# Kernel tuning notes

Hardware: AMD Instinct MI355X
Metric: run time of the kernel (lower is better)

Reference implementation:

```python
import jax, jax.numpy as jnp
import numpy as np

HIDDEN = 768
HEADS = 12
HEAD_DIM = 64
SEQ = 512
DS_K = 64  # downsampling_k
EPS = 1e-6


def setup_inputs() -> dict:
    key = jax.random.key(0)
    ks = jax.random.split(key, 16)
    B = 32
    sd = 1.0 / DS_K
    glorot = jax.nn.initializers.lecun_normal()  # flax default_kernel_init
    inp = {
        "query": jax.random.normal(ks[0], (B, SEQ, HIDDEN), jnp.float32),
        "key": jax.random.normal(ks[1], (B, SEQ, HIDDEN), jnp.float32),
        "value": jax.random.normal(ks[2], (B, SEQ, HIDDEN), jnp.float32),
        "step": 0,
        # learned Linformer-style downsampling projections [k, s]
        "W_kds": sd * jax.random.normal(ks[3], (DS_K, SEQ), jnp.float32),
        "W_vds": sd * jax.random.normal(ks[4], (DS_K, SEQ), jnp.float32),
        # DenseGeneral qkv kernels [d, n, h] and biases [n, h]
        "Wq": glorot(ks[5], (HIDDEN, HEADS, HEAD_DIM), jnp.float32),
        "bq": jnp.zeros((HEADS, HEAD_DIM), jnp.float32),
        "Wk": glorot(ks[6], (HIDDEN, HEADS, HEAD_DIM), jnp.float32),
        "bk": jnp.zeros((HEADS, HEAD_DIM), jnp.float32),
        "Wv": glorot(ks[7], (HIDDEN, HEADS, HEAD_DIM), jnp.float32),
        "bv": jnp.zeros((HEADS, HEAD_DIM), jnp.float32),
        # out projection contracts (n, h) -> hidden
        "Wout": glorot(ks[8], (HEADS * HEAD_DIM, HIDDEN), jnp.float32).reshape(HEADS, HEAD_DIM, HIDDEN),
        "bout": jnp.zeros((HIDDEN,), jnp.float32),
    }
    return inp


def reference(query, key, value, step, W_kds, W_vds, Wq, bq, Wk, bk, Wv, bv, Wout, bout):
    # Linformer-style downsample of keys/values along sequence: [b,s,d] -> [b,k,d]
    key_ds = jnp.einsum("ks,bsd->bkd", W_kds, key)
    val_ds = jnp.einsum("ks,bsd->bkd", W_vds, value)

    # per-head projections
    queries = jnp.einsum("bqd,dnh->bqnh", query, Wq) + bq    # [b,q,n,h]
    keys = jnp.einsum("bkd,dnh->bknh", key_ds, Wk) + bk      # [b,k,n,h]
    values = jnp.einsum("bkd,dnh->bknh", val_ds, Wv) + bv    # [b,k,n,h]

    # kernelized linear attention with elu feature map (mask=False path)
    phi_q = jax.nn.elu(queries) + 1.0
    phi_k = jax.nn.elu(keys) + 1.0
    s = jnp.einsum("bknd,bknh->bndh", phi_k, values)          # [b,n,h,h] KV state
    z = jnp.sum(phi_k, axis=1)                                 # [b,n,h]
    qs = jnp.einsum("bqnd,bndh->bqnh", phi_q, s)
    qz = jnp.einsum("bqnd,bnd->bqn", phi_q, z) + EPS
    a_v = qs / qz[..., None]                                   # [b,q,n,h]

    out = jnp.einsum("bqnh,nhD->bqD", a_v, Wout) + bout        # [b,q,hidden]
    return out
```

## Files before the change

### kernel.cpp

```cpp
#include <hip/hip_runtime.h>

typedef unsigned short u16;
typedef u16 u16x4 __attribute__((ext_vector_type(4)));
typedef u16 u16x8 __attribute__((ext_vector_type(8)));
typedef __bf16 bf16;
typedef bf16 bf16x8 __attribute__((ext_vector_type(8)));
typedef float f32x4 __attribute__((ext_vector_type(4)));

__device__ __forceinline__ float bf2f(u16 v) {
  union { unsigned u; float f; } x; x.u = ((unsigned)v) << 16; return x.f;
}
__device__ __forceinline__ u16 f2bf(float f) {
  union { float f; unsigned u; } x; x.f = f;
  unsigned u = x.u;
  u += 0x7fffu + ((u >> 16) & 1u);
  return (u16)(u >> 16);
}
__device__ __forceinline__ unsigned cvt2bf(float lo, float hi) {
  unsigned r;
  asm("v_cvt_pk_bf16_f32 %0, %1, %2" : "=v"(r) : "v"(lo), "v"(hi));
  return r;
}

__device__ __forceinline__ void bar_lgkm() {
  asm volatile("s_waitcnt lgkmcnt(0)" ::: "memory");
  __builtin_amdgcn_s_barrier();
}

#define GLDS16(g, l) __builtin_amdgcn_global_load_lds( \
    (const __attribute__((address_space(1))) unsigned int*)(const void*)(g), \
    (__attribute__((address_space(3))) unsigned int*)(void*)(l), 16, 0, 0)

__global__ __launch_bounds__(256) void prepds_k(
    const float* __restrict__ Wq, const float* __restrict__ Wk,
    const float* __restrict__ Wv, const float* __restrict__ Wout,
    const float* __restrict__ query,
    const float* __restrict__ W_kds, const float* __restrict__ W_vds,
    const float* __restrict__ b0, const float* __restrict__ b1,
    const float* __restrict__ b2, const float* __restrict__ b3,
    const float* __restrict__ key, const float* __restrict__ value,
    u16* __restrict__ WT, u16* __restrict__ q_bf,
    u16* __restrict__ dstB, u16* __restrict__ key_ds)
{
  __shared__ char sm[10240];
  const int blk = blockIdx.x;
  const int t = threadIdx.x;

  if (blk % 10 == 0) {
    u16* Bs = (u16*)sm;
    const int id = blk / 10;
    const int nt = (id % 12) * 64;
    const int yb = id / 12;
    const int pair = yb >> 5, b = yb & 31;
    const float* src = (pair ? value : key) + (size_t)b * 512 * 768;
    const float* W32 = pair ? W_vds : W_kds;
    u16* dst = key_ds + (size_t)pair * 1572864 + (size_t)b * 49152;
    const int wave = t >> 6, lane = t & 63;
    const int wm = (wave >> 1) * 32, wn = (wave & 1) * 32;
    const int lrow = lane & 15, quad = lane >> 4;
    const int bn = t & 63, bk8 = (t >> 6) * 8;
    const float* bcol = src + nt + bn;

    auto ldW = [&](int row, int kq) -> bf16x8 {
      f32x4 w0 = *(const f32x4*)&W32[(size_t)row * 512 + kq];
      f32x4 w1 = *(const f32x4*)&W32[(size_t)row * 512 + kq + 4];
      union { unsigned u[4]; bf16x8 v; } cv;
      cv.u[0] = cvt2bf(w0[0], w0[1]); cv.u[1] = cvt2bf(w0[2], w0[3]);
      cv.u[2] = cvt2bf(w1[0], w1[1]); cv.u[3] = cvt2bf(w1[2], w1[3]);
      return cv.v;
    };

    f32x4 acc[2][2] = {};
    float breg[8];
    bf16x8 av[2][2];

    #pragma unroll
    for (int i = 0; i < 8; ++i) breg[i] = bcol[(size_t)(bk8 + i) * 768];
    #pragma unroll
    for (int i = 0; i < 2; ++i) av[0][i] = ldW(wm + i * 16 + lrow, quad * 8);

    #pragma unroll
    for (int step = 0; step < 16; ++step) {
      const int cur = step & 1, nxt = cur ^ 1;
      u16x8 wv;
      #pragma unroll
      for (int i = 0; i < 8; ++i) wv[i] = f2bf(breg[i]);
      *(u16x8*)&Bs[cur * 2560 + bn * 40 + bk8] = wv;
      if (step < 15) {
        const int k1 = (step + 1) * 32;
        #pragma unroll
        for (int i = 0; i < 8; ++i) breg[i] = bcol[(size_t)(k1 + bk8 + i) * 768];
        #pragma unroll
        for (int i = 0; i < 2; ++i) av[nxt][i] = ldW(wm + i * 16 + lrow, k1 + quad * 8);
      }
      bar_lgkm();
      bf16x8 bv[2];
      #pragma unroll
      for (int j = 0; j < 2; ++j)
        bv[j] = *(const bf16x8*)&Bs[cur * 2560 + (wn + j * 16 + lrow) * 40 + quad * 8];
      #pragma unroll
      for (int i = 0; i < 2; ++i)
        #pragma unroll
        for (int j = 0; j < 2; ++j)
          acc[i][j] = __builtin_amdgcn_mfma_f32_16x16x32_bf16(av[cur][i], bv[j], acc[i][j], 0, 0, 0);
    }

    #pragma unroll
    for (int i = 0; i < 2; ++i)
      #pragma unroll
      for (int j = 0; j < 2; ++j) {
        const int col = nt + wn + j * 16 + lrow;
        #pragma unroll
        for (int r = 0; r < 4; ++r) {
          const int row = wm + i * 16 + quad * 4 + r;
          dst[(size_t)row * 768 + col] = f2bf(acc[i][j][r]);
        }
      }
    return;
  }

  const int pid = blk - blk / 10 - 1;
  if (pid < 576) {
    u16 (*T)[72] = (u16(*)[72])sm;
    const int bz = pid / 144, rr = pid % 144;
    const int r0 = (rr / 12) * 64, c0 = (rr % 12) * 64;
    const float* W = (bz == 0) ? Wq : (bz == 1) ? Wk : (bz == 2) ? Wv : Wout;
    u16* O = WT + (size_t)bz * 768 * 768;
    #pragma unroll
    for (int p = 0; p < 2; ++p) {
      int v = t + p * 256;
      int r = v / 8, c = (v % 8) * 8;
      f32x4 x0 = *(const f32x4*)&W[(size_t)(r0 + r) * 768 + c0 + c];
      f32x4 x1 = *(const f32x4*)&W[(size_t)(r0 + r) * 768 + c0 + c + 4];
      #pragma unroll
      for (int i = 0; i < 4; ++i) { T[r][c + i] = f2bf(x0[i]); T[r][c + 4 + i] = f2bf(x1[i]); }
    }
    __syncthreads();
    #pragma unroll
    for (int p = 0; p < 2; ++p) {
      int v = t + p * 256;
      int r = v / 8, c = (v % 8) * 8;
      u16x8 tv;
      #pragma unroll
      for (int i = 0; i < 8; ++i) tv[i] = T[c + i][r];
      *(u16x8*)&O[(size_t)(c0 + r) * 768 + r0 + c] = tv;
    }
  } else if (pid < 6720) {
    const size_t i = (size_t)(pid - 576) * 256 + t;
    f32x4 a = *(const f32x4*)&query[i * 8];
    f32x4 b = *(const f32x4*)&query[i * 8 + 4];
    u16x8 w;
    #pragma unroll
    for (int j = 0; j < 4; ++j) { w[j] = f2bf(a[j]); w[4 + j] = f2bf(b[j]); }
    *(u16x8*)&q_bf[i * 8] = w;
  } else if (pid < 6732) {
    const int i = (pid - 6720) * 256 + t;
    if (i < 3072) {
      int s = i / 768, si = i % 768;
      const float* src = (s == 0) ? b0 : (s == 1) ? b1 : (s == 2) ? b2 : b3;
      dstB[i] = f2bf(src[si]);
    }
  }
}

template<int ACT, bool OF32>
__global__ __launch_bounds__(256) void gemm64_k(
    const u16* __restrict__ A, int lda,
    const u16* __restrict__ Bt, int ldb,
    void* __restrict__ Craw, int ldc,
    const u16* __restrict__ bias, int K)
{
  __shared__ u16 As[128 * 64];
  __shared__ u16 Bs[128 * 64];
  const int blk = blockIdx.x;
  const int wg = (blk & 7) * 96 + (blk >> 3);
  const int mt = (wg / 6) * 128, nt = (wg % 6) * 128;
  const int t = threadIdx.x, wave = t >> 6, lane = t & 63;
  const int wm = (wave >> 1) * 64, wn = (wave & 1) * 64;
  const int lrow = lane & 15, quad = lane >> 4;
  f32x4 acc[4][4] = {};

  for (int k0 = 0; k0 < K; k0 += 64) {
    __syncthreads();
    #pragma unroll
    for (int p = 0; p < 4; ++p) {
      const int slot = wave * 256 + p * 64 + lane;
      const int r = slot >> 3, ch = slot & 7;
      const int chs = ch ^ (r & 7);
      const int lb = (wave * 256 + p * 64) * 8;
      GLDS16(&A[(size_t)(mt + r) * lda + k0 + chs * 8], &As[lb]);
      GLDS16(&Bt[(size_t)(nt + r) * ldb + k0 + chs * 8], &Bs[lb]);
    }
    __syncthreads();

    #pragma unroll
    for (int c = 0; c < 2; ++c) {
      bf16x8 av[4], bv[4];
      #pragma unroll
      for (int i = 0; i < 4; ++i) {
        const int row = wm + i * 16 + lrow;
        av[i] = *(const bf16x8*)&As[row * 64 + (((c * 4 + quad) ^ (row & 7)) * 8)];
      }
      #pragma unroll
      for (int j = 0; j < 4; ++j) {
        const int row = wn + j * 16 + lrow;
        bv[j] = *(const bf16x8*)&Bs[row * 64 + (((c * 4 + quad) ^ (row & 7)) * 8)];
      }
      #pragma unroll
      for (int i = 0; i < 4; ++i)
        #pragma unroll
        for (int j = 0; j < 4; ++j)
          acc[i][j] = __builtin_amdgcn_mfma_f32_16x16x32_bf16(av[i], bv[j], acc[i][j], 0, 0, 0);
    }
  }

  #pragma unroll
  for (int i = 0; i < 4; ++i) {
    #pragma unroll
    for (int j = 0; j < 4; ++j) {
      const int col = nt + wn + j * 16 + lrow;
      const float badd = bias ? bf2f(bias[col]) : 0.0f;
      #pragma unroll
      for (int r = 0; r < 4; ++r) {
        const int row = mt + wm + i * 16 + quad * 4 + r;
        float v = acc[i][j][r] + badd;
        if constexpr (ACT == 1) v = v > 0.0f ? v + 1.0f : __expf(v);
        if constexpr (OF32) ((float*)Craw)[(size_t)row * ldc + col] = v;
        else                ((u16*)Craw)[(size_t)row * ldc + col] = f2bf(v);
      }
    }
  }
}

__global__ __launch_bounds__(256) void fkv_k(
    const u16* __restrict__ key_ds,
    const u16* __restrict__ WT,
    const u16* __restrict__ bias_c,
    u16* __restrict__ sT, float* __restrict__ z)
{
  __shared__ char sm[32768];
  u16* T0 = (u16*)sm;
  u16* Pt = (u16*)sm;
  u16* Vt = (u16*)(sm + 9216);
  const int x = blockIdx.x;
  const int b = x / 12, n = x % 12;
  const int t = threadIdx.x, wave = t >> 6, lane = t & 63;
  const u16* srcs[4] = {
    key_ds + (size_t)b * 49152,
    WT + 589824 + (size_t)n * 49152,
    key_ds + 1572864 + (size_t)b * 49152,
    WT + 2 * 589824 + (size_t)n * 49152 };
  const int grow = lane >> 3;
  const int gchunk = (lane & 7) ^ (grow & 7);
  const int isV = wave & 1;
  const int wm = (wave >> 1) * 32;
  u16* Atile = T0 + (isV ? 2 : 0) * 4096;
  u16* Btile = T0 + (isV ? 3 : 1) * 4096;
  const int lrow = lane & 15, quad = lane >> 4;
  f32x4 acc[2][4] = {};

  for (int k0 = 0; k0 < 768; k0 += 64) {
    const u16* s = srcs[wave];
    u16* dtile = T0 + wave * 4096;
    #pragma unroll
    for (int j = 0; j < 8; ++j) {
      const u16* gsrc = s + (size_t)(j * 8 + grow) * 768 + k0 + gchunk * 8;
      GLDS16(gsrc, (char*)dtile + j * 1024);
    }
    __syncthreads();
    #pragma unroll
    for (int c = 0; c < 2; ++c) {
      bf16x8 av[2], bv[4];
      #pragma unroll
      for (int i = 0; i < 2; ++i) {
        const int row = wm + i * 16 + lrow;
        av[i] = *(const bf16x8*)&Atile[row * 64 + (((c * 4 + quad) ^ (row & 7)) * 8)];
      }
      #pragma unroll
      for (int j = 0; j < 4; ++j) {
        const int row = j * 16 + lrow;
        bv[j] = *(const bf16x8*)&Btile[row * 64 + (((c * 4 + quad) ^ (row & 7)) * 8)];
      }
      #pragma unroll
      for (int i = 0; i < 2; ++i)
        #pragma unroll
        for (int j = 0; j < 4; ++j)
          acc[i][j] = __builtin_amdgcn_mfma_f32_16x16x32_bf16(av[i], bv[j], acc[i][j], 0, 0, 0);
    }
    __syncthreads();
  }

  const u16* bias = bias_c + (isV ? 1536 : 768) + n * 64;
  u16* Ttile = isV ? Vt : Pt;
  #pragma unroll
  for (int i = 0; i < 2; ++i)
    #pragma unroll
    for (int j = 0; j < 4; ++j) {
      const int col = j * 16 + lrow;
      const float badd = bf2f(bias[col]);
      u16x4 pk4;
      #pragma unroll
      for (int r = 0; r < 4; ++r) {
        float v = acc[i][j][r] + badd;
        if (!isV) v = v > 0.0f ? v + 1.0f : __expf(v);
        pk4[r] = f2bf(v);
      }
      *(u16x4*)&Ttile[col * 72 + wm + i * 16 + quad * 4] = pk4;
    }
  __syncthreads();

  const int wm2 = (wave >> 1) * 32, wn2 = (wave & 1) * 32;
  f32x4 a2[2][2] = {};
  #pragma unroll
  for (int c = 0; c < 2; ++c) {
    bf16x8 av[2], bv[2];
    #pragma unroll
    for (int i = 0; i < 2; ++i)
      av[i] = *(const bf16x8*)&Vt[(wm2 + i * 16 + lrow) * 72 + c * 32 + quad * 8];
    #pragma unroll
    for (int j = 0; j < 2; ++j)
      bv[j] = *(const bf16x8*)&Pt[(wn2 + j * 16 + lrow) * 72 + c * 32 + quad * 8];
    #pragma unroll
    for (int i = 0; i < 2; ++i)
      #pragma unroll
      for (int j = 0; j < 2; ++j)
        a2[i][j] = __builtin_amdgcn_mfma_f32_16x16x32_bf16(av[i], bv[j], a2[i][j], 0, 0, 0);
  }
  u16* sTg = sT + (size_t)x * 4096;
  #pragma unroll
  for (int i = 0; i < 2; ++i)
    #pragma unroll
    for (int j = 0; j < 2; ++j)
      #pragma unroll
      for (int r = 0; r < 4; ++r)
        sTg[(size_t)(wm2 + i * 16 + quad * 4 + r) * 64 + wn2 + j * 16 + lrow] = f2bf(a2[i][j][r]);
  if (t < 64) {
    float zz = 0.f;
    #pragma unroll
    for (int g = 0; g < 8; ++g) {
      u16x8 p = *(const u16x8*)&Pt[t * 72 + g * 8];
      #pragma unroll
      for (int e = 0; e < 8; ++e) zz += bf2f(p[e]);
    }
    z[(size_t)x * 64 + t] = zz;
  }
}

__global__ __launch_bounds__(256) void attn_av_k(
    u16* __restrict__ phi_q, const u16* __restrict__ sT, const float* __restrict__ zbuf)
{
  __shared__ u16 As[64 * 72];
  __shared__ u16 Bs[64 * 72];
  __shared__ float zv[64];
  __shared__ float zpart[4][64];
  __shared__ float zq[64];
  const int x = blockIdx.x, y = blockIdx.y;
  const int b = y / 12, n = y % 12;
  const int t = threadIdx.x;
  u16* Abase = phi_q + (size_t)b * 512 * 768 + (size_t)x * 64 * 768 + n * 64;
  const u16* Bbase = sT + (size_t)y * 4096;
  if (t < 64) zv[t] = zbuf[(size_t)y * 64 + t];
  #pragma unroll
  for (int p = 0; p < 2; ++p) {
    int v = t + p * 256;
    int r = v >> 3, c = (v & 7) * 8;
    *(u16x8*)&As[r * 72 + c] = *(const u16x8*)&Abase[(size_t)r * 768 + c];
    *(u16x8*)&Bs[r * 72 + c] = *(const u16x8*)&Bbase[r * 64 + c];
  }
  __syncthreads();
  {
    int r = t & 63, seg = t >> 6;
    float s = 0.f;
    #pragma unroll
    for (int j = 0; j < 16; ++j) s += bf2f(As[r * 72 + seg * 16 + j]) * zv[seg * 16 + j];
    zpart[seg][r] = s;
  }
  __syncthreads();
  if (t < 64) {
    float s = zpart[0][t] + zpart[1][t] + zpart[2][t] + zpart[3][t];
    zq[t] = 1.0f / (s + 1e-6f);
  }
  const int wave = t >> 6, lane = t & 63;
  const int wm = (wave >> 1) * 32, wn = (wave & 1) * 32;
  const int lrow = lane & 15, quad = lane >> 4;
  f32x4 acc[2][2] = {};
  #pragma unroll
  for (int c = 0; c < 2; ++c) {
    bf16x8 av[2], bv[2];
    #pragma unroll
    for (int i = 0; i < 2; ++i) av[i] = *(const bf16x8*)&As[(wm + i * 16 + lrow) * 72 + c * 32 + quad * 8];
    #pragma unroll
    for (int j = 0; j < 2; ++j) bv[j] = *(const bf16x8*)&Bs[(wn + j * 16 + lrow) * 72 + c * 32 + quad * 8];
    #pragma unroll
    for (int i = 0; i < 2; ++i)
      #pragma unroll
      for (int j = 0; j < 2; ++j)
        acc[i][j] = __builtin_amdgcn_mfma_f32_16x16x32_bf16(av[i], bv[j], acc[i][j], 0, 0, 0);
  }
  __syncthreads();
  #pragma unroll
  for (int i = 0; i < 2; ++i)
    #pragma unroll
    for (int j = 0; j < 2; ++j) {
      const int col = wn + j * 16 + lrow;
      #pragma unroll
      for (int r = 0; r < 4; ++r) {
        const int row = wm + i * 16 + quad * 4 + r;
        Abase[(size_t)row * 768 + col] = f2bf(acc[i][j][r] * zq[row]);
      }
    }
}

__global__ void tagfill_k(float* out, float val, int n) {
  int i = blockIdx.x * 256 + threadIdx.x;
  if (i < n) out[i] = val;
}

extern "C" void kernel_launch(void* const* d_in, const int* in_sizes, int n_in,
                              void* d_out, int out_size, void* d_ws, size_t ws_size,
                              hipStream_t stream) {
  (void)out_size;
  float* out = (float*)d_out;

  int o;
  if (n_in >= 14 && in_sizes[3] == 1) o = 4;
  else if (n_in == 13) o = 3;
  else { tagfill_k<<<4, 256, 0, stream>>>(out, 77.0f, 1024); return; }
  if (in_sizes[0] != 12582912 || in_sizes[o + 0] != 32768 || in_sizes[o + 2] != 589824) {
    tagfill_k<<<4, 256, 0, stream>>>(out, 88.0f, 1024); return;
  }

  const float* query = (const float*)d_in[0];
  const float* key   = (const float*)d_in[1];
  const float* value = (const float*)d_in[2];
  const float* W_kds = (const float*)d_in[o + 0];
  const float* W_vds = (const float*)d_in[o + 1];
  const float* Wq   = (const float*)d_in[o + 2];
  const float* bq   = (const float*)d_in[o + 3];
  const float* Wk   = (const float*)d_in[o + 4];
  const float* bk   = (const float*)d_in[o + 5];
  const float* Wv   = (const float*)d_in[o + 6];
  const float* bv   = (const float*)d_in[o + 7];
  const float* Wout = (const float*)d_in[o + 8];
  const float* bout = (const float*)d_in[o + 9];

  const size_t NEED = 61478912;
  if (ws_size < NEED) { tagfill_k<<<4, 256, 0, stream>>>(out, 123.0f, 1024); return; }

  char* base = (char*)d_ws;
  u16*   WT     = (u16*)base;
  char*  Breg   = base + 4718592;
  u16*   q_bf   = (u16*)Breg;
  u16*   sT     = (u16*)Breg;
  float* zbuf   = (float*)(Breg + 3145728);
  u16*   phi_q  = (u16*)(base + 29884416);
  u16*   bias_c = (u16*)(base + 55181312);
  u16*   key_ds = (u16*)(base + 55187456);
  u16* a_v = phi_q;
  u16* WqT   = WT;
  u16* WoutT = WT + 3 * 768 * 768;
  u16* bq_c = bias_c, *bout_c = bias_c + 2304;

  prepds_k<<<7680, 256, 0, stream>>>(Wq, Wk, Wv, Wout, query, W_kds, W_vds,
                                     bq, bk, bv, bout, key, value,
                                     WT, q_bf, bias_c, key_ds);

  gemm64_k<1, false><<<768, 256, 0, stream>>>(
      q_bf, 768, WqT, 768, phi_q, 768, bq_c, 768);

  fkv_k<<<384, 256, 0, stream>>>(key_ds, WT, bias_c, sT, zbuf);

  attn_av_k<<<dim3(8, 384), 256, 0, stream>>>(phi_q, sT, zbuf);

  gemm64_k<0, true><<<768, 256, 0, stream>>>(
      a_v, 768, WoutT, 768, out, 768, bout_c, 768);
}
```

Baseline: 319.7 us.

## Split sequence downsampling into its own kernel with smaller tiles and bf16 weights

```diff
diff --git a/kernel.cpp b/kernel.cpp
--- a/kernel.cpp
+++ b/kernel.cpp
@@ -16,11 +16,6 @@
   u += 0x7fffu + ((u >> 16) & 1u);
   return (u16)(u >> 16);
 }
-__device__ __forceinline__ unsigned cvt2bf(float lo, float hi) {
-  unsigned r;
-  asm("v_cvt_pk_bf16_f32 %0, %1, %2" : "=v"(r) : "v"(lo), "v"(hi));
-  return r;
-}
 
 __device__ __forceinline__ void bar_lgkm() {
   asm volatile("s_waitcnt lgkmcnt(0)" ::: "memory");
@@ -31,98 +26,21 @@
     (const __attribute__((address_space(1))) unsigned int*)(const void*)(g), \
     (__attribute__((address_space(3))) unsigned int*)(void*)(l), 16, 0, 0)
 
-__global__ __launch_bounds__(256) void prepds_k(
+__global__ __launch_bounds__(256) void prep_k(
     const float* __restrict__ Wq, const float* __restrict__ Wk,
     const float* __restrict__ Wv, const float* __restrict__ Wout,
     const float* __restrict__ query,
-    const float* __restrict__ W_kds, const float* __restrict__ W_vds,
+    const float* __restrict__ wkds, const float* __restrict__ wvds,
     const float* __restrict__ b0, const float* __restrict__ b1,
     const float* __restrict__ b2, const float* __restrict__ b3,
-    const float* __restrict__ key, const float* __restrict__ value,
     u16* __restrict__ WT, u16* __restrict__ q_bf,
-    u16* __restrict__ dstB, u16* __restrict__ key_ds)
+    u16* __restrict__ dstW, u16* __restrict__ dstB)
 {
-  __shared__ char sm[10240];
+  __shared__ u16 T[64][72];
   const int blk = blockIdx.x;
   const int t = threadIdx.x;
-
-  if (blk % 10 == 0) {
-    u16* Bs = (u16*)sm;
-    const int id = blk / 10;
-    const int nt = (id % 12) * 64;
-    const int yb = id / 12;
-    const int pair = yb >> 5, b = yb & 31;
-    const float* src = (pair ? value : key) + (size_t)b * 512 * 768;
-    const float* W32 = pair ? W_vds : W_kds;
-    u16* dst = key_ds + (size_t)pair * 1572864 + (size_t)b * 49152;
-    const int wave = t >> 6, lane = t & 63;
-    const int wm = (wave >> 1) * 32, wn = (wave & 1) * 32;
-    const int lrow = lane & 15, quad = lane >> 4;
-    const int bn = t & 63, bk8 = (t >> 6) * 8;
-    const float* bcol = src + nt + bn;
-
-    auto ldW = [&](int row, int kq) -> bf16x8 {
-      f32x4 w0 = *(const f32x4*)&W32[(size_t)row * 512 + kq];
-      f32x4 w1 = *(const f32x4*)&W32[(size_t)row * 512 + kq + 4];
-      union { unsigned u[4]; bf16x8 v; } cv;
-      cv.u[0] = cvt2bf(w0[0], w0[1]); cv.u[1] = cvt2bf(w0[2], w0[3]);
-      cv.u[2] = cvt2bf(w1[0], w1[1]); cv.u[3] = cvt2bf(w1[2], w1[3]);
-      return cv.v;
-    };
-
-    f32x4 acc[2][2] = {};
-    float breg[8];
-    bf16x8 av[2][2];
-
-    #pragma unroll
-    for (int i = 0; i < 8; ++i) breg[i] = bcol[(size_t)(bk8 + i) * 768];
-    #pragma unroll
-    for (int i = 0; i < 2; ++i) av[0][i] = ldW(wm + i * 16 + lrow, quad * 8);
-
-    #pragma unroll
-    for (int step = 0; step < 16; ++step) {
-      const int cur = step & 1, nxt = cur ^ 1;
-      u16x8 wv;
-      #pragma unroll
-      for (int i = 0; i < 8; ++i) wv[i] = f2bf(breg[i]);
-      *(u16x8*)&Bs[cur * 2560 + bn * 40 + bk8] = wv;
-      if (step < 15) {
-        const int k1 = (step + 1) * 32;
-        #pragma unroll
-        for (int i = 0; i < 8; ++i) breg[i] = bcol[(size_t)(k1 + bk8 + i) * 768];
-        #pragma unroll
-        for (int i = 0; i < 2; ++i) av[nxt][i] = ldW(wm + i * 16 + lrow, k1 + quad * 8);
-      }
-      bar_lgkm();
-      bf16x8 bv[2];
-      #pragma unroll
-      for (int j = 0; j < 2; ++j)
-        bv[j] = *(const bf16x8*)&Bs[cur * 2560 + (wn + j * 16 + lrow) * 40 + quad * 8];
-      #pragma unroll
-      for (int i = 0; i < 2; ++i)
-        #pragma unroll
-        for (int j = 0; j < 2; ++j)
-          acc[i][j] = __builtin_amdgcn_mfma_f32_16x16x32_bf16(av[cur][i], bv[j], acc[i][j], 0, 0, 0);
-    }
-
-    #pragma unroll
-    for (int i = 0; i < 2; ++i)
-      #pragma unroll
-      for (int j = 0; j < 2; ++j) {
-        const int col = nt + wn + j * 16 + lrow;
-        #pragma unroll
-        for (int r = 0; r < 4; ++r) {
-          const int row = wm + i * 16 + quad * 4 + r;
-          dst[(size_t)row * 768 + col] = f2bf(acc[i][j][r]);
-        }
-      }
-    return;
-  }
-
-  const int pid = blk - blk / 10 - 1;
-  if (pid < 576) {
-    u16 (*T)[72] = (u16(*)[72])sm;
-    const int bz = pid / 144, rr = pid % 144;
+  if (blk < 576) {
+    const int bz = blk / 144, rr = blk % 144;
     const int r0 = (rr / 12) * 64, c0 = (rr % 12) * 64;
     const float* W = (bz == 0) ? Wq : (bz == 1) ? Wk : (bz == 2) ? Wv : Wout;
     u16* O = WT + (size_t)bz * 768 * 768;
@@ -145,20 +63,81 @@
       for (int i = 0; i < 8; ++i) tv[i] = T[c + i][r];
       *(u16x8*)&O[(size_t)(c0 + r) * 768 + r0 + c] = tv;
     }
-  } else if (pid < 6720) {
-    const size_t i = (size_t)(pid - 576) * 256 + t;
+  } else if (blk < 6720) {
+    const size_t i = (size_t)(blk - 576) * 256 + t;
     f32x4 a = *(const f32x4*)&query[i * 8];
     f32x4 b = *(const f32x4*)&query[i * 8 + 4];
     u16x8 w;
     #pragma unroll
     for (int j = 0; j < 4; ++j) { w[j] = f2bf(a[j]); w[4 + j] = f2bf(b[j]); }
     *(u16x8*)&q_bf[i * 8] = w;
-  } else if (pid < 6732) {
-    const int i = (pid - 6720) * 256 + t;
-    if (i < 3072) {
-      int s = i / 768, si = i % 768;
+  } else {
+    const int i = (blk - 6720) * 256 + t;
+    if (i < 32768)      dstW[i] = f2bf(wkds[i]);
+    else if (i < 65536) dstW[i] = f2bf(wvds[i - 32768]);
+    else {
+      int j = i - 65536, s = j / 768, si = j % 768;
       const float* src = (s == 0) ? b0 : (s == 1) ? b1 : (s == 2) ? b2 : b3;
-      dstB[i] = f2bf(src[si]);
+      dstB[j] = f2bf(src[si]);
+    }
+  }
+}
+
+__global__ __launch_bounds__(256) void ds_k(
+    const u16* __restrict__ Wds,
+    const float* __restrict__ key, const float* __restrict__ value,
+    u16* __restrict__ key_ds)
+{
+  __shared__ u16 Bs[2][32 * 40];
+  const int pair = blockIdx.y >> 5, b = blockIdx.y & 31;
+  const float* src = (pair ? value : key) + (size_t)b * 512 * 768;
+  const u16* W = Wds + pair * 32768;
+  u16* dst = key_ds + (size_t)pair * 1572864 + (size_t)b * 49152;
+  const int nt = blockIdx.x * 32;
+  const int t = threadIdx.x, wave = t >> 6, lane = t & 63;
+  const int wm = wave * 16;
+  const int lrow = lane & 15, quad = lane >> 4;
+  const int bn = t & 31, bk4 = (t >> 5) * 4;
+  const float* bcol = src + nt + bn;
+
+  f32x4 acc[2] = {};
+  float breg[4];
+  bf16x8 av[2];
+
+  #pragma unroll
+  for (int i = 0; i < 4; ++i) breg[i] = bcol[(size_t)(bk4 + i) * 768];
+  av[0] = *(const bf16x8*)&W[(size_t)(wm + lrow) * 512 + quad * 8];
+
+  #pragma unroll
+  for (int step = 0; step < 16; ++step) {
+    const int cur = step & 1, nxt = cur ^ 1;
+    u16x4 wv;
+    #pragma unroll
+    for (int i = 0; i < 4; ++i) wv[i] = f2bf(breg[i]);
+    *(u16x4*)&Bs[cur][bn * 40 + bk4] = wv;
+    if (step < 15) {
+      const int k1 = (step + 1) * 32;
+      #pragma unroll
+      for (int i = 0; i < 4; ++i) breg[i] = bcol[(size_t)(k1 + bk4 + i) * 768];
+      av[nxt] = *(const bf16x8*)&W[(size_t)(wm + lrow) * 512 + k1 + quad * 8];
+    }
+    bar_lgkm();
+    bf16x8 bv[2];
+    #pragma unroll
+    for (int j = 0; j < 2; ++j)
+      bv[j] = *(const bf16x8*)&Bs[cur][(j * 16 + lrow) * 40 + quad * 8];
+    #pragma unroll
+    for (int j = 0; j < 2; ++j)
+      acc[j] = __builtin_amdgcn_mfma_f32_16x16x32_bf16(av[cur], bv[j], acc[j], 0, 0, 0);
+  }
+
+  #pragma unroll
+  for (int j = 0; j < 2; ++j) {
+    const int col = nt + j * 16 + lrow;
+    #pragma unroll
+    for (int r = 0; r < 4; ++r) {
+      const int row = wm + quad * 4 + r;
+      dst[(size_t)row * 768 + col] = f2bf(acc[j][r]);
     }
   }
 }
@@ -454,6 +433,7 @@
   u16*   sT     = (u16*)Breg;
   float* zbuf   = (float*)(Breg + 3145728);
   u16*   phi_q  = (u16*)(base + 29884416);
+  u16*   Wds_c  = (u16*)(base + 55050240);
   u16*   bias_c = (u16*)(base + 55181312);
   u16*   key_ds = (u16*)(base + 55187456);
   u16* a_v = phi_q;
@@ -461,13 +441,14 @@
   u16* WoutT = WT + 3 * 768 * 768;
   u16* bq_c = bias_c, *bout_c = bias_c + 2304;
 
-  prepds_k<<<7680, 256, 0, stream>>>(Wq, Wk, Wv, Wout, query, W_kds, W_vds,
-                                     bq, bk, bv, bout, key, value,
-                                     WT, q_bf, bias_c, key_ds);
+  prep_k<<<6988, 256, 0, stream>>>(Wq, Wk, Wv, Wout, query, W_kds, W_vds,
+                                   bq, bk, bv, bout, WT, q_bf, Wds_c, bias_c);
 
   gemm64_k<1, false><<<768, 256, 0, stream>>>(
       q_bf, 768, WqT, 768, phi_q, 768, bq_c, 768);
 
+  ds_k<<<dim3(24, 64), 256, 0, stream>>>(Wds_c, key, value, key_ds);
+
   fkv_k<<<384, 256, 0, stream>>>(key_ds, WT, bias_c, sT, zbuf);
 
   attn_av_k<<<dim3(8, 384), 256, 0, stream>>>(phi_q, sT, zbuf);
```

Result: faster. 298.9 us (-6.5%).
